# Kernel optimization log

Measured on AMD Instinct MI355X. Metric: run time of the kernel, lower is better.

The kernel has to match this reference:

```python
import jax, jax.numpy as jnp
import numpy as np

B, N, D = 64, 197, 768
H, E, R = 12, 8, 8


def setup_inputs() -> dict:
    key = jax.random.key(0)
    ks = jax.random.split(key, 8)
    s = 0.02
    return {
        "tokens": jax.random.normal(ks[0], (B, N, D), dtype=jnp.float32),
        "qkv_w": jax.random.normal(ks[1], (3 * D, D), dtype=jnp.float32) * s,
        "qkv_b": jax.random.normal(ks[2], (3 * D,), dtype=jnp.float32) * s,
        "proj_w": jax.random.normal(ks[3], (D, D), dtype=jnp.float32) * s,
        "proj_b": jax.random.normal(ks[4], (D,), dtype=jnp.float32) * s,
        "gate_w": jax.random.normal(ks[5], (E, D), dtype=jnp.float32) * s,
        "lora_a": jax.random.normal(ks[6], (E, D, R), dtype=jnp.float32) * s,
        "lora_b": jax.random.normal(ks[7], (E, R, 3 * D), dtype=jnp.float32) * s,
    }


def reference(tokens, qkv_w, qkv_b, proj_w, proj_b, gate_w, lora_a, lora_b):
    b, n, d = tokens.shape
    hd = d // H
    scale = hd ** (-0.5)
    # frozen qkv projection: [b, n, 3d]
    qkv = jnp.einsum("bnd,kd->bnk", tokens, qkv_w) + qkv_b
    # LoRA-MoE delta (soft router over experts)
    gates = jax.nn.softmax(jnp.einsum("bnd,ed->bne", tokens, gate_w), axis=-1)
    h = jnp.einsum("bnd,edr->bner", tokens, lora_a)  # [b,n,E,R]
    delta = jnp.einsum("bner,erk,bne->bnk", h, lora_b, gates)  # [b,n,3d]
    # adding delta before the reshape is identical to per-q/k/v addition after
    qkv = (qkv + delta).reshape(b, n, 3, H, hd).transpose(2, 0, 3, 1, 4)
    q, k, v = qkv[0], qkv[1], qkv[2]  # each [b,H,n,hd]
    attn = jax.nn.softmax(jnp.einsum("bhqd,bhkd->bhqk", q, k) * scale, axis=-1)
    out = jnp.einsum("bhqk,bhkd->bhqd", attn, v)
    out = out.transpose(0, 2, 1, 3).reshape(b, n, d)
    return jnp.einsum("bnd,kd->bnk", out, proj_w) + proj_b
```

## Files before the change

kernel.cpp:

```cpp
#include <hip/hip_runtime.h>
#include <hip/hip_bf16.h>

typedef __hip_bfloat16 BF16;
typedef __attribute__((ext_vector_type(8))) short bf16x8;
typedef __attribute__((ext_vector_type(4))) short bf16x4;
typedef __attribute__((ext_vector_type(4))) float f32x4;
typedef __attribute__((ext_vector_type(4))) int int4v;
typedef __attribute__((ext_vector_type(2))) int int2v;

#define MTOK 12608
#define D_IN 768
#define KAUG 832
#define N_QKV 2304

#define AS1 __attribute__((address_space(1)))
#define AS3 __attribute__((address_space(3)))
#define SB0() __builtin_amdgcn_sched_barrier(0)

#if __has_builtin(__builtin_amdgcn_mfma_f32_16x16x16bf16_1k)
__device__ __forceinline__ f32x4 mfma16(bf16x4 a, bf16x4 b, f32x4 c) {
  return __builtin_amdgcn_mfma_f32_16x16x16bf16_1k(a, b, c, 0, 0, 0);
}
#else
__device__ __forceinline__ f32x4 mfma16(bf16x4 a, bf16x4 b, f32x4 c) {
  f32x4 d;
  asm volatile("v_mfma_f32_16x16x16_bf16 %0, %1, %2, %3"
               : "=v"(d) : "v"(a), "v"(b), "0"(c));
  return d;
}
#endif

__global__ __launch_bounds__(256) void prep_waug_k(const float* __restrict__ qkv_w,
                                                   const float* __restrict__ lora_b,
                                                   BF16* __restrict__ Waug) {
  int idx = blockIdx.x*256 + threadIdx.x;
  if (idx >= N_QKV*KAUG) return;
  int k = idx / KAUG, c = idx - k*KAUG;
  float v = (c < D_IN) ? qkv_w[k*D_IN + c] : lora_b[(size_t)(c - D_IN)*N_QKV + k];
  Waug[idx] = (BF16)v;
}

__global__ __launch_bounds__(256) void prep_pb_k(const float* __restrict__ proj_w,
                                                 BF16* __restrict__ Pb) {
  int idx = blockIdx.x*256 + threadIdx.x;
  if (idx < D_IN*D_IN) Pb[idx] = (BF16)proj_w[idx];
}

__global__ __launch_bounds__(256) void prep_lat_k(const float* __restrict__ lora_a,
                                                  BF16* __restrict__ LAt) {
  int idx = blockIdx.x*256 + threadIdx.x;
  if (idx >= 64*D_IN) return;
  int j = idx / D_IN, d = idx - j*D_IN;
  LAt[idx] = (BF16)lora_a[(size_t)(j >> 3)*6144 + d*8 + (j & 7)];
}

__global__ __launch_bounds__(256) void token_prep_k(const float* __restrict__ tokens,
                                                    const float* __restrict__ gate_w,
                                                    BF16* __restrict__ Aaug,
                                                    float* __restrict__ gates) {
  int w = blockIdx.x*4 + (threadIdx.x >> 6);
  int lane = threadIdx.x & 63;
  if (w >= MTOK) return;
  const float4* x4 = (const float4*)(tokens + (size_t)w*D_IN);
  float4 xv[3];
  #pragma unroll
  for (int i=0;i<3;++i) xv[i] = x4[lane + 64*i];
  #pragma unroll
  for (int i=0;i<3;++i) {
    ushort4 u;
    BF16 b0 = (BF16)xv[i].x, b1 = (BF16)xv[i].y, b2 = (BF16)xv[i].z, b3 = (BF16)xv[i].w;
    u.x = *(unsigned short*)&b0; u.y = *(unsigned short*)&b1;
    u.z = *(unsigned short*)&b2; u.w = *(unsigned short*)&b3;
    *(ushort4*)(Aaug + (size_t)w*KAUG + (lane + 64*i)*4) = u;
  }
  float g[8] = {0,0,0,0,0,0,0,0};
  #pragma unroll
  for (int i=0;i<3;++i) {
    const int d4 = (lane + 64*i)*4;
    #pragma unroll
    for (int e=0;e<8;++e) {
      float4 gw = *(const float4*)(gate_w + e*D_IN + d4);
      g[e] += xv[i].x*gw.x + xv[i].y*gw.y + xv[i].z*gw.z + xv[i].w*gw.w;
    }
  }
  #pragma unroll
  for (int e=0;e<8;++e) {
    #pragma unroll
    for (int off=32; off; off >>= 1) g[e] += __shfl_xor(g[e], off);
  }
  float mx = g[0];
  #pragma unroll
  for (int e=1;e<8;++e) mx = fmaxf(mx, g[e]);
  float pe[8]; float ssum = 0.f;
  #pragma unroll
  for (int e=0;e<8;++e) { pe[e] = __expf(g[e]-mx); ssum += pe[e]; }
  float inv = 1.f/ssum;
  if (lane < 8) {
    float val = 0.f;
    #pragma unroll
    for (int e=0;e<8;++e) val = (lane==e) ? pe[e]*inv : val;
    gates[(size_t)w*8 + lane] = val;
  }
}

template<int ROWS>
__device__ __forceinline__ void stage_bt(const BF16* __restrict__ g, int ldg, int row0, int M,
                                         BF16* lds, int kbase, int t) {
  constexpr int NIT = ROWS*8/256;
  #pragma unroll
  for (int it=0; it<NIT; ++it) {
    int c = it*256 + t;
    int r = c >> 3, kc = c & 7;
    int rg = row0 + r;
    rg = (rg < M) ? rg : (M-1);
    const BF16* gp = g + (size_t)rg*ldg + kbase + kc*8;
    BF16* lp = lds + (it*256 + (t & ~63))*8;
    __builtin_amdgcn_global_load_lds((const AS1 void*)gp, (AS3 void*)lp, 16, 0, 0);
  }
}

template<int BM, int BN, int EPI>
__global__ __launch_bounds__(256,3) void gemm_bt_k(const BF16* __restrict__ A, int lda,
                                                   const BF16* __restrict__ Bt, int ldb,
                                                   const float* __restrict__ aux,
                                                   void* __restrict__ Cv, int ldc,
                                                   int M, int K) {
  constexpr int BK = 64;
  constexpr int WM = BM/2, WN = BN/2;
  constexpr int MF = WM/16, NF = WN/16;
  __shared__ BF16 Al[BM*BK];
  __shared__ BF16 Bl[BN*BK];
  const int n0 = blockIdx.x*BN, m0 = blockIdx.y*BM;
  const int t = threadIdx.x, lane = t & 63, wid = t >> 6;
  const int wm = (wid >> 1)*WM, wn = (wid & 1)*WN;
  f32x4 acc[MF][NF] = {};
  const int KT = K/BK;
  for (int kt=0; kt<KT; ++kt) {
    stage_bt<BM>(A, lda, m0, M, Al, kt*BK, t);
    stage_bt<BN>(Bt, ldb, n0, 1<<30, Bl, kt*BK, t);
    __syncthreads();
    #pragma unroll
    for (int kk=0; kk<2; ++kk) {
      bf16x8 a[MF], b[NF];
      const int col = kk*32 + (lane >> 4)*8;
      #pragma unroll
      for (int m=0;m<MF;++m) a[m] = *(const bf16x8*)(Al + (wm + m*16 + (lane & 15))*BK + col);
      #pragma unroll
      for (int n=0;n<NF;++n) b[n] = *(const bf16x8*)(Bl + (wn + n*16 + (lane & 15))*BK + col);
      #pragma unroll
      for (int m=0;m<MF;++m)
        #pragma unroll
        for (int n=0;n<NF;++n)
          acc[m][n] = __builtin_amdgcn_mfma_f32_16x16x32_bf16(a[m], b[n], acc[m][n], 0, 0, 0);
    }
    __syncthreads();
  }
  #pragma unroll
  for (int m=0;m<MF;++m) {
    #pragma unroll
    for (int n=0;n<NF;++n) {
      const int rb = m0 + wm + m*16 + (lane >> 4)*4;
      const int c = n0 + wn + n*16 + (lane & 15);
      #pragma unroll
      for (int j=0;j<4;++j) {
        const int r = rb + j;
        if (r < M) {
          float v = acc[m][n][j];
          if (EPI == 0) {
            v *= aux[(size_t)r*8 + (c >> 3)];
            ((BF16*)Cv)[(size_t)r*ldc + c] = (BF16)v;
          } else if (EPI == 1) {
            v += aux[c];
            ((BF16*)Cv)[(size_t)r*ldc + c] = (BF16)v;
          } else {
            v += aux[c];
            ((float*)Cv)[(size_t)r*ldc + c] = v;
          }
        }
      }
    }
  }
}

template<int EPI, int NBN, int LDA, int LDB, int LDC>
__global__ __launch_bounds__(256,2) void gemm2_k(const BF16* __restrict__ A,
                                                 const BF16* __restrict__ Bt,
                                                 const float* __restrict__ bias,
                                                 void* __restrict__ Cv,
                                                 int M, int K) {
  __shared__ BF16 Lsh[2][2][8192];
  const int t = threadIdx.x, lane = t & 63, wid = t >> 6;
  const int nwg = gridDim.x;
  const int q8 = nwg >> 3, r8 = nwg & 7;
  const int xcd = blockIdx.x & 7, pos = blockIdx.x >> 3;
  const int wg = (xcd < r8 ? xcd*(q8+1) : r8*(q8+1) + (xcd - r8)*q8) + pos;
  const int mb = wg / NBN, nb = wg - mb*NBN;
  const int m0 = mb*128, n0 = nb*128;
  const int KT = K/64;
  const int q4 = lane & 15;
  const int wm = (wid >> 1)*64, wn = (wid & 1)*64;

  const BF16 *sA[4], *sB[4];
  #pragma unroll
  for (int it=0; it<4; ++it) {
    int c = it*256 + t;
    int r = c >> 3, p = c & 7;
    int sc = p ^ (r & 7);
    int ra = m0 + r; ra = ra < M ? ra : M-1;
    sA[it] = A  + (size_t)ra*LDA + sc*8;
    sB[it] = Bt + (size_t)(n0 + r)*LDB + sc*8;
  }
  auto stageAB = [&](int buf, int tile) {
    #pragma unroll
    for (int it=0; it<4; ++it)
      __builtin_amdgcn_global_load_lds((const AS1 void*)(sA[it] + tile*64),
        (AS3 void*)(&Lsh[buf][0][0] + (it*256 + (t & ~63))*8), 16, 0, 0);
    #pragma unroll
    for (int it=0; it<4; ++it)
      __builtin_amdgcn_global_load_lds((const AS1 void*)(sB[it] + tile*64),
        (AS3 void*)(&Lsh[buf][1][0] + (it*256 + (t & ~63))*8), 16, 0, 0);
  };

  const int sw = (q4 & 7) << 3;
  const int ck[2] = { (((lane >> 4)*8)) ^ sw, ((32 + (lane >> 4)*8)) ^ sw };

  f32x4 acc[4][4] = {};
  stageAB(0, 0);
  asm volatile("s_waitcnt vmcnt(0)" ::: "memory"); SB0();
  __builtin_amdgcn_s_barrier();

  for (int kt = 0; kt < KT; ++kt) {
    const int buf = kt & 1;
    if (kt+1 < KT) stageAB(buf^1, kt+1);
    bf16x8 a[4][2], b[4][2];
    #pragma unroll
    for (int m=0;m<4;++m)
      #pragma unroll
      for (int kk=0;kk<2;++kk)
        a[m][kk] = *(const bf16x8*)(&Lsh[buf][0][0] + (wm + m*16 + q4)*64 + ck[kk]);
    #pragma unroll
    for (int n=0;n<4;++n)
      #pragma unroll
      for (int kk=0;kk<2;++kk)
        b[n][kk] = *(const bf16x8*)(&Lsh[buf][1][0] + (wn + n*16 + q4)*64 + ck[kk]);
    asm volatile("s_waitcnt lgkmcnt(0)" ::: "memory"); SB0();
    __builtin_amdgcn_s_setprio(1);
    #pragma unroll
    for (int kk=0;kk<2;++kk)
      #pragma unroll
      for (int m=0;m<4;++m)
        #pragma unroll
        for (int n=0;n<4;++n)
          acc[m][n] = __builtin_amdgcn_mfma_f32_16x16x32_bf16(a[m][kk], b[n][kk], acc[m][n], 0,0,0);
    __builtin_amdgcn_s_setprio(0);
    SB0();
    if (kt+1 < KT) asm volatile("s_waitcnt vmcnt(0)" ::: "memory");
    SB0();
    __builtin_amdgcn_s_barrier();
  }

  float bv[4];
  #pragma unroll
  for (int n=0;n<4;++n) bv[n] = bias[n0 + wn + n*16 + q4];
  #pragma unroll
  for (int m=0;m<4;++m) {
    #pragma unroll
    for (int j=0;j<4;++j) {
      const int r = m0 + wm + m*16 + (lane >> 4)*4 + j;
      if (r < M) {
        #pragma unroll
        for (int n=0;n<4;++n) {
          float v = acc[m][n][j] + bv[n];
          const size_t idx = (size_t)r*LDC + n0 + wn + n*16 + q4;
          if (EPI == 1) ((BF16*)Cv)[idx] = (BF16)v;
          else          ((float*)Cv)[idx] = v;
        }
      }
    }
  }
}

__device__ __forceinline__ int pack2bf(float lo, float hi) {
  BF16 a = (BF16)lo, b = (BF16)hi;
  unsigned short al = *(unsigned short*)&a, bh = *(unsigned short*)&b;
  return (int)(((unsigned)bh << 16) | (unsigned)al);
}

__global__ __launch_bounds__(256,2) void attn_k(const BF16* __restrict__ QKV,
                                                BF16* __restrict__ O) {
  constexpr int KSTR = 72;
  constexpr int VSTR = 236;
  constexpr int OSTR = 72;
  __shared__ BF16 Kl[208*KSTR];
  __shared__ BF16 Vt[64*VSTR];
  __shared__ BF16 Ol[4][16*OSTR];
  const int bh = blockIdx.x;
  const int b = bh / 12, h = bh - b*12;
  const size_t rowbase = (size_t)b*197;
  const int t = threadIdx.x, lane = t & 63, wid = t >> 6;
  const BF16 z = (BF16)0.0f;
  int4v rk[7], rv[7];
  int cc[7];
  #pragma unroll
  for (int it=0; it<7; ++it) {
    int c = t + it*256; c = (c < 1663) ? c : 1663;
    cc[it] = c;
    int r = c >> 3, kc = c & 7;
    int rr = (r < 197) ? r : 196;
    rk[it] = *(const int4v*)(QKV + (rowbase + rr)*N_QKV + 768  + h*64 + kc*8);
    rv[it] = *(const int4v*)(QKV + (rowbase + rr)*N_QKV + 1536 + h*64 + kc*8);
  }
  #pragma unroll
  for (int it=0; it<7; ++it) {
    int c = cc[it];
    int r = c >> 3, kc = c & 7;
    int4v kval = rk[it];
    if (r >= 197) { kval[0]=0; kval[1]=0; kval[2]=0; kval[3]=0; }
    *(int4v*)(Kl + r*KSTR + kc*8) = kval;
    const BF16* pv = (const BF16*)&rv[it];
    if (r < 197) {
      #pragma unroll
      for (int i=0;i<8;++i) Vt[(kc*8 + i)*VSTR + r] = pv[i];
    } else {
      #pragma unroll
      for (int i=0;i<8;++i) Vt[(kc*8 + i)*VSTR + r] = z;
    }
  }
  __syncthreads();

  const int g = lane >> 4;
  const int q4 = lane & 15;

  for (int chunk = wid; chunk < 13; chunk += 4) {
    const int q0 = chunk*16;
    int qr = q0 + q4;
    qr = (qr < 197) ? qr : 196;
    bf16x8 qa[2];
    #pragma unroll
    for (int kk=0;kk<2;++kk)
      qa[kk] = *(const bf16x8*)(QKV + (rowbase + qr)*N_QKV + h*64 + kk*32 + g*8);
    f32x4 zf = {0.f,0.f,0.f,0.f};
    f32x4 s[13];
    #pragma unroll
    for (int nf=0;nf<13;++nf) s[nf] = zf;
    #pragma unroll
    for (int nf=0;nf<13;++nf) {
      #pragma unroll
      for (int kk=0;kk<2;++kk) {
        bf16x8 kb = *(const bf16x8*)(Kl + (nf*16 + q4)*KSTR + kk*32 + g*8);
        s[nf] = __builtin_amdgcn_mfma_f32_16x16x32_bf16(kb, qa[kk], s[nf], 0, 0, 0);
      }
    }
    float m = -1e30f;
    #pragma unroll
    for (int nf=0;nf<13;++nf) {
      #pragma unroll
      for (int j=0;j<4;++j) {
        const int kg = nf*16 + g*4 + j;
        float v = s[nf][j]*0.125f;
        v = (kg < 197) ? v : -1e30f;
        s[nf][j] = v;
        m = fmaxf(m, v);
      }
    }
    m = fmaxf(m, __shfl_xor(m, 16));
    m = fmaxf(m, __shfl_xor(m, 32));
    float lsum = 0.f;
    #pragma unroll
    for (int nf=0;nf<13;++nf) {
      #pragma unroll
      for (int j=0;j<4;++j) {
        float p = __expf(s[nf][j] - m);
        s[nf][j] = p;
        lsum += p;
      }
    }
    lsum += __shfl_xor(lsum, 16);
    lsum += __shfl_xor(lsum, 32);
    bf16x4 pa[13];
    #pragma unroll
    for (int nf=0;nf<13;++nf) {
      int2v pr;
      pr[0] = pack2bf(s[nf][0], s[nf][1]);
      pr[1] = pack2bf(s[nf][2], s[nf][3]);
      pa[nf] = *(bf16x4*)&pr;
    }
    f32x4 o[4] = {};
    #pragma unroll
    for (int nf=0; nf<13; ++nf) {
      #pragma unroll
      for (int df=0; df<4; ++df) {
        bf16x4 vb = *(const bf16x4*)(Vt + (df*16 + q4)*VSTR + nf*16 + g*4);
        o[df] = mfma16(pa[nf], vb, o[df]);
      }
    }
    float ldiv[4];
    #pragma unroll
    for (int j=0;j<4;++j) ldiv[j] = __shfl(lsum, g*4 + j);
    asm volatile("s_waitcnt lgkmcnt(0)" ::: "memory"); SB0();
    #pragma unroll
    for (int df=0; df<4; ++df)
      #pragma unroll
      for (int j=0;j<4;++j)
        Ol[wid][(g*4 + j)*OSTR + df*16 + q4] = (BF16)(o[df][j] / ldiv[j]);
    asm volatile("s_waitcnt lgkmcnt(0)" ::: "memory"); SB0();
    #pragma unroll
    for (int it=0; it<2; ++it) {
      const int lr = (lane >> 3) + it*8;
      const int chk = lane & 7;
      const int r = q0 + lr;
      int4v v = *(const int4v*)(&Ol[wid][lr*OSTR + chk*8]);
      if (r < 197)
        *(int4v*)(O + (rowbase + r)*768 + h*64 + chk*8) = v;
    }
  }
}

extern "C" void kernel_launch(void* const* d_in, const int* in_sizes, int n_in,
                              void* d_out, int out_size, void* d_ws, size_t ws_size,
                              hipStream_t stream) {
  const float* tokens = (const float*)d_in[0];
  const float* qkv_w  = (const float*)d_in[1];
  const float* qkv_b  = (const float*)d_in[2];
  const float* proj_w = (const float*)d_in[3];
  const float* proj_b = (const float*)d_in[4];
  const float* gate_w = (const float*)d_in[5];
  const float* lora_a = (const float*)d_in[6];
  const float* lora_b = (const float*)d_in[7];

  size_t off = 0;
  auto take = [&](size_t bytes) {
    off = (off + 255) & ~(size_t)255;
    void* p = (char*)d_ws + off;
    off += bytes;
    return p;
  };
  BF16* Waug  = (BF16*)take((size_t)N_QKV*KAUG*2);
  BF16* Pb    = (BF16*)take((size_t)D_IN*D_IN*2);
  BF16* LAt   = (BF16*)take((size_t)64*D_IN*2);
  BF16* Aaug  = (BF16*)take((size_t)MTOK*KAUG*2);
  float* gates= (float*)take((size_t)MTOK*8*4);
  BF16* QKVb  = (BF16*)take((size_t)MTOK*N_QKV*2);
  BF16* Oc    = (BF16*)take((size_t)MTOK*D_IN*2);

  prep_waug_k<<<(N_QKV*KAUG + 255)/256, 256, 0, stream>>>(qkv_w, lora_b, Waug);
  prep_pb_k<<<(D_IN*D_IN + 255)/256, 256, 0, stream>>>(proj_w, Pb);
  prep_lat_k<<<(64*D_IN + 255)/256, 256, 0, stream>>>(lora_a, LAt);
  token_prep_k<<<MTOK/4, 256, 0, stream>>>(tokens, gate_w, Aaug, gates);
  gemm_bt_k<64,64,0><<<dim3(1, MTOK/64), 256, 0, stream>>>(
      Aaug, KAUG, LAt, D_IN, gates, (void*)(Aaug + 768), KAUG, MTOK, D_IN);
  gemm2_k<1, 18, KAUG, KAUG, N_QKV><<<99*18, 256, 0, stream>>>(
      Aaug, Waug, qkv_b, (void*)QKVb, MTOK, KAUG);
  attn_k<<<768, 256, 0, stream>>>(QKVb, Oc);
  gemm2_k<2, 6, D_IN, D_IN, D_IN><<<99*6, 256, 0, stream>>>(
      Oc, Pb, proj_b, d_out, MTOK, D_IN);
}
```

Baseline: 165.0 us.

## Load GEMM B operand directly from global into registers, halve LDS staging

The GEMM kernel no longer stages the weight (B) tile through LDS. Each wave loads its B fragments straight from global memory into registers, while A is still double-buffered in LDS via global_load_lds. LDS use per block is halved, so launch bounds are raised to allow three blocks per CU. Global B reads become strided 16-byte loads duplicated across the two waves sharing an N tile, and the wait counts are split (vmcnt(4)) to overlap the B loads with the A prefetch.

```diff
diff --git a/kernel.cpp b/kernel.cpp
--- a/kernel.cpp
+++ b/kernel.cpp
@@ -183,12 +183,12 @@
 }
 
 template<int EPI, int NBN, int LDA, int LDB, int LDC>
-__global__ __launch_bounds__(256,2) void gemm2_k(const BF16* __restrict__ A,
+__global__ __launch_bounds__(256,3) void gemm3_k(const BF16* __restrict__ A,
                                                  const BF16* __restrict__ Bt,
                                                  const float* __restrict__ bias,
                                                  void* __restrict__ Cv,
                                                  int M, int K) {
-  __shared__ BF16 Lsh[2][2][8192];
+  __shared__ BF16 Ash[2][8192];
   const int t = threadIdx.x, lane = t & 63, wid = t >> 6;
   const int nwg = gridDim.x;
   const int q8 = nwg >> 3, r8 = nwg & 7;
@@ -197,53 +197,62 @@
   const int mb = wg / NBN, nb = wg - mb*NBN;
   const int m0 = mb*128, n0 = nb*128;
   const int KT = K/64;
-  const int q4 = lane & 15;
+  const int q4 = lane & 15, g = lane >> 4;
   const int wm = (wid >> 1)*64, wn = (wid & 1)*64;
 
-  const BF16 *sA[4], *sB[4];
+  const BF16 *sA[4];
   #pragma unroll
   for (int it=0; it<4; ++it) {
     int c = it*256 + t;
     int r = c >> 3, p = c & 7;
     int sc = p ^ (r & 7);
     int ra = m0 + r; ra = ra < M ? ra : M-1;
-    sA[it] = A  + (size_t)ra*LDA + sc*8;
-    sB[it] = Bt + (size_t)(n0 + r)*LDB + sc*8;
-  }
-  auto stageAB = [&](int buf, int tile) {
+    sA[it] = A + (size_t)ra*LDA + sc*8;
+  }
+  auto stageA = [&](int buf, int tile) {
     #pragma unroll
     for (int it=0; it<4; ++it)
       __builtin_amdgcn_global_load_lds((const AS1 void*)(sA[it] + tile*64),
-        (AS3 void*)(&Lsh[buf][0][0] + (it*256 + (t & ~63))*8), 16, 0, 0);
-    #pragma unroll
-    for (int it=0; it<4; ++it)
-      __builtin_amdgcn_global_load_lds((const AS1 void*)(sB[it] + tile*64),
-        (AS3 void*)(&Lsh[buf][1][0] + (it*256 + (t & ~63))*8), 16, 0, 0);
+        (AS3 void*)(&Ash[buf][0] + (it*256 + (t & ~63))*8), 16, 0, 0);
   };
 
+  const BF16* pB[4][2];
+  #pragma unroll
+  for (int n=0;n<4;++n)
+    #pragma unroll
+    for (int kk=0;kk<2;++kk)
+      pB[n][kk] = Bt + (size_t)(n0 + wn + n*16 + q4)*LDB + kk*32 + g*8;
+
   const int sw = (q4 & 7) << 3;
-  const int ck[2] = { (((lane >> 4)*8)) ^ sw, ((32 + (lane >> 4)*8)) ^ sw };
+  const int ck[2] = { ((g*8)) ^ sw, ((32 + g*8)) ^ sw };
 
   f32x4 acc[4][4] = {};
-  stageAB(0, 0);
+  stageA(0, 0);
   asm volatile("s_waitcnt vmcnt(0)" ::: "memory"); SB0();
   __builtin_amdgcn_s_barrier();
 
   for (int kt = 0; kt < KT; ++kt) {
     const int buf = kt & 1;
-    if (kt+1 < KT) stageAB(buf^1, kt+1);
-    bf16x8 a[4][2], b[4][2];
+    const bool nb1 = (kt+1 < KT);
+    bf16x8 bb[4][2];
+    #pragma unroll
+    for (int n=0;n<4;++n)
+      #pragma unroll
+      for (int kk=0;kk<2;++kk)
+        bb[n][kk] = *(const bf16x8*)(pB[n][kk] + kt*64);
+    SB0();
+    if (nb1) stageA(buf^1, kt+1);
+    SB0();
+    bf16x8 aa[4][2];
     #pragma unroll
     for (int m=0;m<4;++m)
       #pragma unroll
       for (int kk=0;kk<2;++kk)
-        a[m][kk] = *(const bf16x8*)(&Lsh[buf][0][0] + (wm + m*16 + q4)*64 + ck[kk]);
-    #pragma unroll
-    for (int n=0;n<4;++n)
-      #pragma unroll
-      for (int kk=0;kk<2;++kk)
-        b[n][kk] = *(const bf16x8*)(&Lsh[buf][1][0] + (wn + n*16 + q4)*64 + ck[kk]);
-    asm volatile("s_waitcnt lgkmcnt(0)" ::: "memory"); SB0();
+        aa[m][kk] = *(const bf16x8*)(&Ash[buf][0] + (wm + m*16 + q4)*64 + ck[kk]);
+    SB0();
+    if (nb1) asm volatile("s_waitcnt vmcnt(4) lgkmcnt(0)" ::: "memory");
+    else     asm volatile("s_waitcnt vmcnt(0) lgkmcnt(0)" ::: "memory");
+    SB0();
     __builtin_amdgcn_s_setprio(1);
     #pragma unroll
     for (int kk=0;kk<2;++kk)
@@ -251,10 +260,10 @@
       for (int m=0;m<4;++m)
         #pragma unroll
         for (int n=0;n<4;++n)
-          acc[m][n] = __builtin_amdgcn_mfma_f32_16x16x32_bf16(a[m][kk], b[n][kk], acc[m][n], 0,0,0);
+          acc[m][n] = __builtin_amdgcn_mfma_f32_16x16x32_bf16(aa[m][kk], bb[n][kk], acc[m][n], 0,0,0);
     __builtin_amdgcn_s_setprio(0);
     SB0();
-    if (kt+1 < KT) asm volatile("s_waitcnt vmcnt(0)" ::: "memory");
+    if (nb1) asm volatile("s_waitcnt vmcnt(0)" ::: "memory");
     SB0();
     __builtin_amdgcn_s_barrier();
   }
@@ -266,7 +275,7 @@
   for (int m=0;m<4;++m) {
     #pragma unroll
     for (int j=0;j<4;++j) {
-      const int r = m0 + wm + m*16 + (lane >> 4)*4 + j;
+      const int r = m0 + wm + m*16 + g*4 + j;
       if (r < M) {
         #pragma unroll
         for (int n=0;n<4;++n) {
@@ -449,9 +458,9 @@
   token_prep_k<<<MTOK/4, 256, 0, stream>>>(tokens, gate_w, Aaug, gates);
   gemm_bt_k<64,64,0><<<dim3(1, MTOK/64), 256, 0, stream>>>(
       Aaug, KAUG, LAt, D_IN, gates, (void*)(Aaug + 768), KAUG, MTOK, D_IN);
-  gemm2_k<1, 18, KAUG, KAUG, N_QKV><<<99*18, 256, 0, stream>>>(
+  gemm3_k<1, 18, KAUG, KAUG, N_QKV><<<99*18, 256, 0, stream>>>(
       Aaug, Waug, qkv_b, (void*)QKVb, MTOK, KAUG);
   attn_k<<<768, 256, 0, stream>>>(QKVb, Oc);
-  gemm2_k<2, 6, D_IN, D_IN, D_IN><<<99*6, 256, 0, stream>>>(
+  gemm3_k<2, 6, D_IN, D_IN, D_IN><<<99*6, 256, 0, stream>>>(
       Oc, Pb, proj_b, d_out, MTOK, D_IN);
 }
```

Result: slower. 229.4 us (+39.0%).
